# Performance work log

Hardware: AMD Instinct MI355X
Metric: run time of the kernel (lower is better)

## Reference

```python
import jax, jax.numpy as jnp
import numpy as np

H = 1024  # hidden_dim; GRU hidden size is H+1, embedding_dim = 2*H


def _bigru_scan(h0, Wih_f, Whh_f, bih_f, bhh_f, Wih_b, Whh_b, bih_b, bhh_b):
    """h0: (T, 2, H+1). Runs the per-token recurrence of AnswerSynthesisEncoder.

    At each step the torch code feeds the previous step's output y (2H+2,) back
    in as the GRU *input* x = y[:2H].reshape(2,H).sum(0), and uses the token
    embedding (+f_s,f_e) reshaped to (2, H+1) as the initial hidden state h_0
    of the bidirectional, seq_len=1 GRU. Since h_0 does not depend on the
    carry, the hidden-side gate preactivations are precomputed as one GEMM.
    """
    Hh = H + 1
    gh_f = h0[:, 0] @ Whh_f.T + bhh_f  # (T, 3*(H+1))
    gh_b = h0[:, 1] @ Whh_b.T + bhh_b

    def cell(x, h, gh, Wih, bih):
        gi = Wih @ x + bih
        i_r, i_z, i_n = jnp.split(gi, 3)
        h_r, h_z, h_n = jnp.split(gh, 3)
        r = jax.nn.sigmoid(i_r + h_r)
        z = jax.nn.sigmoid(i_z + h_z)
        n = jnp.tanh(i_n + r * h_n)
        return (1.0 - z) * n + z * h

    def step(y, inp):
        h0_t, ghf_t, ghb_t = inp
        x = y[: 2 * H].reshape(2, H).sum(axis=0)  # (H,)
        yf = cell(x, h0_t[0], ghf_t, Wih_f, bih_f)
        yb = cell(x, h0_t[1], ghb_t, Wih_b, bih_b)
        y_new = jnp.concatenate([yf, yb])  # (2H+2,)
        return y_new, y_new

    y0 = jnp.zeros(2 * Hh, dtype=h0.dtype)
    _, outs = jax.lax.scan(step, y0, (h0, gh_f, gh_b))  # (T, 2H+2)
    # final slice: reshape(2, H+1)[:, :H] per token -> concat of both halves' first H
    return jnp.concatenate([outs[:, :H], outs[:, Hh : Hh + H]], axis=1)  # (T, 2H)


def setup_inputs() -> dict:
    key = jax.random.key(0)
    ks = jax.random.split(key, 12)
    Hh = H + 1
    s = 0.02
    return {
        "e_q": jax.random.normal(ks[0], (512, 2 * H), jnp.float32),
        "e_p": jax.random.normal(ks[1], (4096, 2 * H), jnp.float32),
        "f_s": jax.random.uniform(ks[2], (4096, 1), jnp.float32),
        "f_e": jax.random.uniform(ks[3], (4096, 1), jnp.float32),
        "Wih_f": jax.random.normal(ks[4], (3 * Hh, H), jnp.float32) * s,
        "Whh_f": jax.random.normal(ks[5], (3 * Hh, Hh), jnp.float32) * s,
        "bih_f": jax.random.normal(ks[6], (3 * Hh,), jnp.float32) * s,
        "bhh_f": jax.random.normal(ks[7], (3 * Hh,), jnp.float32) * s,
        "Wih_b": jax.random.normal(ks[8], (3 * Hh, H), jnp.float32) * s,
        "Whh_b": jax.random.normal(ks[9], (3 * Hh, Hh), jnp.float32) * s,
        "bih_b": jax.random.normal(ks[10], (3 * Hh,), jnp.float32) * s,
        "bhh_b": jax.random.normal(ks[11], (3 * Hh,), jnp.float32) * s,
    }


def reference(e_q, e_p, f_s, f_e, Wih_f, Whh_f, bih_f, bhh_f, Wih_b, Whh_b, bih_b, bhh_b):
    Hh = H + 1
    # h_0 per passage token: cat([e_p_t, f_s_t, f_e_t]).reshape(2, H+1)
    h0_p = jnp.concatenate([e_p, f_s, f_e], axis=1).reshape(-1, 2, Hh)
    # h_0 per query token: cat([e_q_t, 0, 0]).reshape(2, H+1)
    zq = jnp.zeros((e_q.shape[0], 2), e_q.dtype)
    h0_q = jnp.concatenate([e_q, zq], axis=1).reshape(-1, 2, Hh)
    h_p = _bigru_scan(h0_p, Wih_f, Whh_f, bih_f, bhh_f, Wih_b, Whh_b, bih_b, bhh_b)
    h_q = _bigru_scan(h0_q, Wih_f, Whh_f, bih_f, bhh_f, Wih_b, Whh_b, bih_b, bhh_b)
    return (h_q, h_p)
```

## Files before the change

### kernel.cpp

```cpp
#include <hip/hip_runtime.h>
#include <stdint.h>


#define H   1024
#define HH  1025
#define N3  3075
#define TQ  512
#define TP  4096
#define MTOT 4608
#define GTOT 2050

typedef unsigned long long ull;

__device__ __forceinline__ float sigm(float x) { return 1.f / (1.f + __expf(-x)); }

__global__ __launch_bounds__(256, 2) void gh_gemm(
    const float* __restrict__ eq, const float* __restrict__ ep,
    const float* __restrict__ fs, const float* __restrict__ fe,
    const float* __restrict__ Whh_f, const float* __restrict__ bhh_f,
    const float* __restrict__ Whh_b, const float* __restrict__ bhh_b,
    float* __restrict__ ghf, float* __restrict__ ghb)
{
    const int dir = blockIdx.z;
    const float* W  = dir ? Whh_b : Whh_f;
    const float* bh = dir ? bhh_b : bhh_f;
    float* gh = dir ? ghb : ghf;
    const int n0 = blockIdx.x * 128;
    const int m0 = blockIdx.y * 128;

    __shared__ float As[16][132];
    __shared__ float Bs[16][132];

    float acc[8][8];
#pragma unroll
    for (int i = 0; i < 8; i++)
#pragma unroll
        for (int j = 0; j < 8; j++) acc[i][j] = 0.f;

    const int tid = threadIdx.x;
    const int tx = tid & 15, ty = tid >> 4;

    for (int k0 = 0; k0 < HH; k0 += 16) {
#pragma unroll
        for (int u = 0; u < 8; u++) {
            int lin = tid + 256 * u;
            int k = lin & 15;
            int m = lin >> 4;
            int gm = m0 + m;
            int gk = k0 + k;
            float v = 0.f;
            if (gk < HH) {
                bool isq = gm < TQ;
                const float* e = isq ? eq : ep;
                int t = isq ? gm : gm - TQ;
                if (dir == 0)            v = e[(size_t)t * 2048 + gk];
                else if (gk < 1023)      v = e[(size_t)t * 2048 + 1025 + gk];
                else if (!isq)           v = (gk == 1023) ? fs[t] : fe[t];
            }
            As[k][m] = v;
        }
#pragma unroll
        for (int u = 0; u < 8; u++) {
            int lin = tid + 256 * u;
            int k = lin & 15;
            int r = lin >> 4;
            int gr = n0 + r, gk = k0 + k;
            Bs[k][r] = (gr < N3 && gk < HH) ? W[(size_t)gr * HH + gk] : 0.f;
        }
        __syncthreads();
#pragma unroll
        for (int kk = 0; kk < 16; kk++) {
            float4 a0 = *(const float4*)&As[kk][ty * 4];
            float4 a1 = *(const float4*)&As[kk][64 + ty * 4];
            float4 b0 = *(const float4*)&Bs[kk][tx * 4];
            float4 b1 = *(const float4*)&Bs[kk][64 + tx * 4];
            float a[8] = {a0.x, a0.y, a0.z, a0.w, a1.x, a1.y, a1.z, a1.w};
            float b[8] = {b0.x, b0.y, b0.z, b0.w, b1.x, b1.y, b1.z, b1.w};
#pragma unroll
            for (int i = 0; i < 8; i++)
#pragma unroll
                for (int j = 0; j < 8; j++) acc[i][j] += a[i] * b[j];
        }
        __syncthreads();
    }
#pragma unroll
    for (int i = 0; i < 8; i++) {
        int gm = m0 + ((i < 4) ? (ty * 4 + i) : (64 + ty * 4 + i - 4));
#pragma unroll
        for (int j = 0; j < 8; j++) {
            int gr = n0 + ((j < 4) ? (tx * 4 + j) : (64 + tx * 4 + j - 4));
            if (gr < N3) gh[(size_t)gm * N3 + gr] = acc[i][j] + bh[gr];
        }
    }
}

__global__ __launch_bounds__(256, 1) void bigru_scan(
    const float* __restrict__ eq, const float* __restrict__ ep,
    const float* __restrict__ fs, const float* __restrict__ fe,
    const float* __restrict__ Wih_f, const float* __restrict__ bih_f,
    const float* __restrict__ Wih_b, const float* __restrict__ bih_b,
    const float* __restrict__ ghf, const float* __restrict__ ghb,
    ull* __restrict__ comm,
    float* __restrict__ out)
{
    __shared__ float xsh[2][2][1024];

    const int tid  = threadIdx.x;
    const int wave = tid >> 6;
    const int lane = tid & 63;
    const int gbase = blockIdx.x * 12 + wave * 3;

    float wreg[9][16];
    float breg[9];
    int   dre[3], je[3];
    bool  vale[3];
#pragma unroll
    for (int e = 0; e < 3; e++) {
        int g = gbase + e;
        bool v = (g < GTOT);
        int gc = v ? g : 0;
        int dir = gc / HH;
        int j = gc % HH;
        dre[e] = dir; je[e] = j; vale[e] = v;
        const float* Wih = dir ? Wih_b : Wih_f;
        const float* bih = dir ? bih_b : bih_f;
#pragma unroll
        for (int gate = 0; gate < 3; gate++) {
            const float* wr = Wih + (size_t)(gate * HH + j) * H;
#pragma unroll
            for (int i = 0; i < 4; i++) {
                float4 w4 = *(const float4*)(wr + i * 256 + lane * 4);
                wreg[e * 3 + gate][i * 4 + 0] = w4.x;
                wreg[e * 3 + gate][i * 4 + 1] = w4.y;
                wreg[e * 3 + gate][i * 4 + 2] = w4.z;
                wreg[e * 3 + gate][i * 4 + 3] = w4.w;
            }
            breg[e * 3 + gate] = bih[gate * HH + j];
        }
    }

    ull* commP = comm;
    ull* commQ = comm + 2 * GTOT;

    for (int t = 0; t < TP; t++) {
        const bool doq = (t < TQ);
        const int par = t & 1;

        float ghp[9], ghq[9], h0p[3], h0q[3];
#pragma unroll
        for (int e = 0; e < 3; e++) {
            const float* gh = dre[e] ? ghb : ghf;
            const int j = je[e];
            size_t basep = (size_t)(TQ + t) * N3;
            ghp[e * 3 + 0] = gh[basep + 0 * HH + j];
            ghp[e * 3 + 1] = gh[basep + 1 * HH + j];
            ghp[e * 3 + 2] = gh[basep + 2 * HH + j];
            if (dre[e] == 0) h0p[e] = ep[(size_t)t * 2048 + j];
            else h0p[e] = (j < 1023) ? ep[(size_t)t * 2048 + 1025 + j]
                                     : ((j == 1023) ? fs[t] : fe[t]);
            if (doq) {
                size_t baseq = (size_t)t * N3;
                ghq[e * 3 + 0] = gh[baseq + 0 * HH + j];
                ghq[e * 3 + 1] = gh[baseq + 1 * HH + j];
                ghq[e * 3 + 2] = gh[baseq + 2 * HH + j];
                if (dre[e] == 0) h0q[e] = eq[(size_t)t * 2048 + j];
                else h0q[e] = (j < 1023) ? eq[(size_t)t * 2048 + 1025 + j] : 0.f;
            } else { ghq[e*3+0]=ghq[e*3+1]=ghq[e*3+2]=0.f; h0q[e]=0.f; }
        }

        if (t == 0) {
#pragma unroll
            for (int u = 0; u < 4; u++) {
                int j = tid + 256 * u;
                xsh[par][0][j] = 0.f;
                xsh[par][1][j] = 0.f;
            }
        } else {
            const int slot = (t + 1) & 1;
            const unsigned tag = (unsigned)t;
            ull* cp = commP + slot * GTOT;
            ull* cq = commQ + slot * GTOT;
            int idx[8];
#pragma unroll
            for (int u = 0; u < 4; u++) {
                int j = tid + 256 * u;
                idx[2 * u]     = j;
                idx[2 * u + 1] = (j == 0) ? 1024 : (1025 + j - 1);
            }
            ull vp[8], vq[8];
#pragma unroll
            for (int u = 0; u < 8; u++)
                vp[u] = __hip_atomic_load(&cp[idx[u]], __ATOMIC_RELAXED, __HIP_MEMORY_SCOPE_AGENT);
            if (doq) {
#pragma unroll
                for (int u = 0; u < 8; u++)
                    vq[u] = __hip_atomic_load(&cq[idx[u]], __ATOMIC_RELAXED, __HIP_MEMORY_SCOPE_AGENT);
            }
#pragma unroll
            for (int u = 0; u < 8; u++) {
                while ((unsigned)(vp[u] >> 32) != tag) {
                    __builtin_amdgcn_s_sleep(1);
                    vp[u] = __hip_atomic_load(&cp[idx[u]], __ATOMIC_RELAXED, __HIP_MEMORY_SCOPE_AGENT);
                }
            }
#pragma unroll
            for (int u = 0; u < 4; u++) {
                int j = tid + 256 * u;
                xsh[par][0][j] = __uint_as_float((unsigned)vp[2 * u]) +
                                 __uint_as_float((unsigned)vp[2 * u + 1]);
            }
            if (doq) {
#pragma unroll
                for (int u = 0; u < 8; u++) {
                    while ((unsigned)(vq[u] >> 32) != tag) {
                        __builtin_amdgcn_s_sleep(1);
                        vq[u] = __hip_atomic_load(&cq[idx[u]], __ATOMIC_RELAXED, __HIP_MEMORY_SCOPE_AGENT);
                    }
                }
#pragma unroll
                for (int u = 0; u < 4; u++) {
                    int j = tid + 256 * u;
                    xsh[par][1][j] = __uint_as_float((unsigned)vq[2 * u]) +
                                     __uint_as_float((unsigned)vq[2 * u + 1]);
                }
            }
        }
        __syncthreads();

        float accp[9];
        {
            float x[16];
#pragma unroll
            for (int i = 0; i < 4; i++) {
                float4 x4 = *(const float4*)&xsh[par][0][i * 256 + lane * 4];
                x[i * 4 + 0] = x4.x; x[i * 4 + 1] = x4.y;
                x[i * 4 + 2] = x4.z; x[i * 4 + 3] = x4.w;
            }
#pragma unroll
            for (int r = 0; r < 9; r++) {
                float s = 0.f;
#pragma unroll
                for (int i = 0; i < 16; i++) s += wreg[r][i] * x[i];
                accp[r] = s;
            }
        }
#pragma unroll
        for (int r = 0; r < 9; r++) {
            float v = accp[r];
#pragma unroll
            for (int off = 32; off > 0; off >>= 1) v += __shfl_xor(v, off, 64);
            accp[r] = v + breg[r];
        }

        float accq[9];
        if (doq) {
            float x[16];
#pragma unroll
            for (int i = 0; i < 4; i++) {
                float4 x4 = *(const float4*)&xsh[par][1][i * 256 + lane * 4];
                x[i * 4 + 0] = x4.x; x[i * 4 + 1] = x4.y;
                x[i * 4 + 2] = x4.z; x[i * 4 + 3] = x4.w;
            }
#pragma unroll
            for (int r = 0; r < 9; r++) {
                float s = 0.f;
#pragma unroll
                for (int i = 0; i < 16; i++) s += wreg[r][i] * x[i];
#pragma unroll
                for (int off = 32; off > 0; off >>= 1) s += __shfl_xor(s, off, 64);
                accq[r] = s + breg[r];
            }
        }

        const ull tagout = ((ull)(unsigned)(t + 1)) << 32;
#pragma unroll
        for (int e = 0; e < 3; e++) {
            int g = gbase + e;
            {
                float r = sigm(accp[e * 3 + 0] + ghp[e * 3 + 0]);
                float z = sigm(accp[e * 3 + 1] + ghp[e * 3 + 1]);
                float n = tanhf(accp[e * 3 + 2] + r * ghp[e * 3 + 2]);
                float y = (1.f - z) * n + z * h0p[e];
                if (lane == 0 && vale[e]) {
                    ull pk = tagout | (ull)__float_as_uint(y);
                    __hip_atomic_store(&commP[(t & 1) * GTOT + g], pk,
                                       __ATOMIC_RELAXED, __HIP_MEMORY_SCOPE_AGENT);
                    if (je[e] < H)
                        out[(size_t)TQ * 2048 + (size_t)t * 2048 + dre[e] * H + je[e]] = y;
                }
            }
            if (doq) {
                float r = sigm(accq[e * 3 + 0] + ghq[e * 3 + 0]);
                float z = sigm(accq[e * 3 + 1] + ghq[e * 3 + 1]);
                float n = tanhf(accq[e * 3 + 2] + r * ghq[e * 3 + 2]);
                float y = (1.f - z) * n + z * h0q[e];
                if (lane == 0 && vale[e]) {
                    ull pk = tagout | (ull)__float_as_uint(y);
                    __hip_atomic_store(&commQ[(t & 1) * GTOT + g], pk,
                                       __ATOMIC_RELAXED, __HIP_MEMORY_SCOPE_AGENT);
                    if (je[e] < H)
                        out[(size_t)t * 2048 + dre[e] * H + je[e]] = y;
                }
            }
        }
    }
}

extern "C" void kernel_launch(void* const* d_in, const int* in_sizes, int n_in,
                              void* d_out, int out_size, void* d_ws, size_t ws_size,
                              hipStream_t stream) {
    const float* eq    = (const float*)d_in[0];
    const float* ep    = (const float*)d_in[1];
    const float* fs    = (const float*)d_in[2];
    const float* fe    = (const float*)d_in[3];
    const float* Wih_f = (const float*)d_in[4];
    const float* Whh_f = (const float*)d_in[5];
    const float* bih_f = (const float*)d_in[6];
    const float* bhh_f = (const float*)d_in[7];
    const float* Wih_b = (const float*)d_in[8];
    const float* Whh_b = (const float*)d_in[9];
    const float* bih_b = (const float*)d_in[10];
    const float* bhh_b = (const float*)d_in[11];
    float* out = (float*)d_out;

    const size_t ghElems = (size_t)MTOT * N3;
    float* ghf = (float*)d_ws;
    float* ghb = ghf + ghElems;
    size_t commOff = ((2 * ghElems * sizeof(float)) + 4095) & ~(size_t)4095;
    ull* comm = (ull*)((char*)d_ws + commOff);

    hipMemsetAsync(comm, 0, (size_t)4 * GTOT * sizeof(ull), stream);

    dim3 ggrid((N3 + 127) / 128, MTOT / 128, 2);
    gh_gemm<<<ggrid, 256, 0, stream>>>(eq, ep, fs, fe, Whh_f, bhh_f, Whh_b, bhh_b, ghf, ghb);

    bigru_scan<<<dim3(171), dim3(256), 0, stream>>>(
        eq, ep, fs, fe, Wih_f, bih_f, Wih_b, bih_b, ghf, ghb, comm, out);
}
```

Before: 16.66 ms.

## Prefetch next-step gate inputs, merge spin-waits, use fast tanh in GRU scan

Loads the precomputed hidden-gate preactivations and h0 values for step t+1 during step t, so global-load latency overlaps the matvec instead of sitting on the serial critical path. The per-element offsets become wave-uniform scalars via readfirstlane. The P and Q spin-waits are merged into one polling loop without s_sleep, the output stores are moved after both communication stores, and tanhf is replaced by an exp-based fast tanh. This trades some register pressure and a small amount of tanh accuracy (overflow handling for large inputs) for lower per-step latency.

```diff
diff --git a/kernel.cpp b/kernel.cpp
--- a/kernel.cpp
+++ b/kernel.cpp
@@ -9,10 +9,15 @@
 #define TP  4096
 #define MTOT 4608
 #define GTOT 2050
+#define GH_ELEMS (MTOT * N3)
 
 typedef unsigned long long ull;
 
 __device__ __forceinline__ float sigm(float x) { return 1.f / (1.f + __expf(-x)); }
+__device__ __forceinline__ float fast_tanh(float x) {
+    float e = __expf(2.f * x);
+    return (e - 1.f) / (e + 1.f);
+}
 
 __global__ __launch_bounds__(256, 2) void gh_gemm(
     const float* __restrict__ eq, const float* __restrict__ ep,
@@ -139,34 +144,49 @@
         }
     }
 
+    int sgh[3], sh0[3], sspec[3];
+#pragma unroll
+    for (int e = 0; e < 3; e++) {
+        sgh[e]   = __builtin_amdgcn_readfirstlane(dre[e] * GH_ELEMS + je[e]);
+        sh0[e]   = __builtin_amdgcn_readfirstlane(dre[e] ? (1025 + je[e]) : je[e]);
+        sspec[e] = __builtin_amdgcn_readfirstlane(
+                       (dre[e] && je[e] >= 1023) ? (je[e] - 1022) : 0);
+    }
+    const float* ghAll = ghf;
+
+    float ghcP[9], h0cP[3], ghcQ[9], h0cQ[3];
+
+    auto loadP = [&](int tt, float gh9[9], float h03[3]) {
+        size_t base = (size_t)(TQ + tt) * N3;
+#pragma unroll
+        for (int e = 0; e < 3; e++) {
+#pragma unroll
+            for (int gate = 0; gate < 3; gate++)
+                gh9[e * 3 + gate] = ghAll[base + (size_t)sgh[e] + gate * HH];
+            h03[e] = (sspec[e] == 0) ? ep[(size_t)tt * 2048 + sh0[e]]
+                   : (sspec[e] == 1) ? fs[tt] : fe[tt];
+        }
+    };
+    auto loadQ = [&](int tt, float gh9[9], float h03[3]) {
+        size_t base = (size_t)tt * N3;
+#pragma unroll
+        for (int e = 0; e < 3; e++) {
+#pragma unroll
+            for (int gate = 0; gate < 3; gate++)
+                gh9[e * 3 + gate] = ghAll[base + (size_t)sgh[e] + gate * HH];
+            h03[e] = (sspec[e] == 0) ? eq[(size_t)tt * 2048 + sh0[e]] : 0.f;
+        }
+    };
+
+    loadP(0, ghcP, h0cP);
+    loadQ(0, ghcQ, h0cQ);
+
     ull* commP = comm;
     ull* commQ = comm + 2 * GTOT;
 
     for (int t = 0; t < TP; t++) {
         const bool doq = (t < TQ);
         const int par = t & 1;
-
-        float ghp[9], ghq[9], h0p[3], h0q[3];
-#pragma unroll
-        for (int e = 0; e < 3; e++) {
-            const float* gh = dre[e] ? ghb : ghf;
-            const int j = je[e];
-            size_t basep = (size_t)(TQ + t) * N3;
-            ghp[e * 3 + 0] = gh[basep + 0 * HH + j];
-            ghp[e * 3 + 1] = gh[basep + 1 * HH + j];
-            ghp[e * 3 + 2] = gh[basep + 2 * HH + j];
-            if (dre[e] == 0) h0p[e] = ep[(size_t)t * 2048 + j];
-            else h0p[e] = (j < 1023) ? ep[(size_t)t * 2048 + 1025 + j]
-                                     : ((j == 1023) ? fs[t] : fe[t]);
-            if (doq) {
-                size_t baseq = (size_t)t * N3;
-                ghq[e * 3 + 0] = gh[baseq + 0 * HH + j];
-                ghq[e * 3 + 1] = gh[baseq + 1 * HH + j];
-                ghq[e * 3 + 2] = gh[baseq + 2 * HH + j];
-                if (dre[e] == 0) h0q[e] = eq[(size_t)t * 2048 + j];
-                else h0q[e] = (j < 1023) ? eq[(size_t)t * 2048 + 1025 + j] : 0.f;
-            } else { ghq[e*3+0]=ghq[e*3+1]=ghq[e*3+2]=0.f; h0q[e]=0.f; }
-        }
 
         if (t == 0) {
 #pragma unroll
@@ -196,11 +216,24 @@
                 for (int u = 0; u < 8; u++)
                     vq[u] = __hip_atomic_load(&cq[idx[u]], __ATOMIC_RELAXED, __HIP_MEMORY_SCOPE_AGENT);
             }
-#pragma unroll
-            for (int u = 0; u < 8; u++) {
-                while ((unsigned)(vp[u] >> 32) != tag) {
-                    __builtin_amdgcn_s_sleep(1);
-                    vp[u] = __hip_atomic_load(&cp[idx[u]], __ATOMIC_RELAXED, __HIP_MEMORY_SCOPE_AGENT);
+            bool done = false;
+            while (!done) {
+                done = true;
+#pragma unroll
+                for (int u = 0; u < 8; u++) {
+                    if ((unsigned)(vp[u] >> 32) != tag) {
+                        done = false;
+                        vp[u] = __hip_atomic_load(&cp[idx[u]], __ATOMIC_RELAXED, __HIP_MEMORY_SCOPE_AGENT);
+                    }
+                }
+                if (doq) {
+#pragma unroll
+                    for (int u = 0; u < 8; u++) {
+                        if ((unsigned)(vq[u] >> 32) != tag) {
+                            done = false;
+                            vq[u] = __hip_atomic_load(&cq[idx[u]], __ATOMIC_RELAXED, __HIP_MEMORY_SCOPE_AGENT);
+                        }
+                    }
                 }
             }
 #pragma unroll
@@ -211,13 +244,6 @@
             }
             if (doq) {
 #pragma unroll
-                for (int u = 0; u < 8; u++) {
-                    while ((unsigned)(vq[u] >> 32) != tag) {
-                        __builtin_amdgcn_s_sleep(1);
-                        vq[u] = __hip_atomic_load(&cq[idx[u]], __ATOMIC_RELAXED, __HIP_MEMORY_SCOPE_AGENT);
-                    }
-                }
-#pragma unroll
                 for (int u = 0; u < 4; u++) {
                     int j = tid + 256 * u;
                     xsh[par][1][j] = __uint_as_float((unsigned)vq[2 * u]) +
@@ -227,6 +253,12 @@
         }
         __syncthreads();
 
+        float ghnP[9], h0nP[3], ghnQ[9], h0nQ[3];
+        const bool ldn = (t + 1) < TP;
+        const bool ldq = (t + 1) < TQ;
+        if (ldn) loadP(t + 1, ghnP, h0nP);
+        if (ldq) loadQ(t + 1, ghnQ, h0nQ);
+
         float accp[9];
         {
             float x[16];
@@ -273,35 +305,55 @@
         }
 
         const ull tagout = ((ull)(unsigned)(t + 1)) << 32;
+        float yP[3], yQ[3];
 #pragma unroll
         for (int e = 0; e < 3; e++) {
-            int g = gbase + e;
-            {
-                float r = sigm(accp[e * 3 + 0] + ghp[e * 3 + 0]);
-                float z = sigm(accp[e * 3 + 1] + ghp[e * 3 + 1]);
-                float n = tanhf(accp[e * 3 + 2] + r * ghp[e * 3 + 2]);
-                float y = (1.f - z) * n + z * h0p[e];
+            float r = sigm(accp[e * 3 + 0] + ghcP[e * 3 + 0]);
+            float z = sigm(accp[e * 3 + 1] + ghcP[e * 3 + 1]);
+            float n = fast_tanh(accp[e * 3 + 2] + r * ghcP[e * 3 + 2]);
+            yP[e] = (1.f - z) * n + z * h0cP[e];
+            if (lane == 0 && vale[e]) {
+                ull pk = tagout | (ull)__float_as_uint(yP[e]);
+                __hip_atomic_store(&commP[par * GTOT + (gbase + e)], pk,
+                                   __ATOMIC_RELAXED, __HIP_MEMORY_SCOPE_AGENT);
+            }
+        }
+        if (doq) {
+#pragma unroll
+            for (int e = 0; e < 3; e++) {
+                float r = sigm(accq[e * 3 + 0] + ghcQ[e * 3 + 0]);
+                float z = sigm(accq[e * 3 + 1] + ghcQ[e * 3 + 1]);
+                float n = fast_tanh(accq[e * 3 + 2] + r * ghcQ[e * 3 + 2]);
+                yQ[e] = (1.f - z) * n + z * h0cQ[e];
                 if (lane == 0 && vale[e]) {
-                    ull pk = tagout | (ull)__float_as_uint(y);
-                    __hip_atomic_store(&commP[(t & 1) * GTOT + g], pk,
+                    ull pk = tagout | (ull)__float_as_uint(yQ[e]);
+                    __hip_atomic_store(&commQ[par * GTOT + (gbase + e)], pk,
                                        __ATOMIC_RELAXED, __HIP_MEMORY_SCOPE_AGENT);
-                    if (je[e] < H)
-                        out[(size_t)TQ * 2048 + (size_t)t * 2048 + dre[e] * H + je[e]] = y;
-                }
-            }
-            if (doq) {
-                float r = sigm(accq[e * 3 + 0] + ghq[e * 3 + 0]);
-                float z = sigm(accq[e * 3 + 1] + ghq[e * 3 + 1]);
-                float n = tanhf(accq[e * 3 + 2] + r * ghq[e * 3 + 2]);
-                float y = (1.f - z) * n + z * h0q[e];
-                if (lane == 0 && vale[e]) {
-                    ull pk = tagout | (ull)__float_as_uint(y);
-                    __hip_atomic_store(&commQ[(t & 1) * GTOT + g], pk,
-                                       __ATOMIC_RELAXED, __HIP_MEMORY_SCOPE_AGENT);
-                    if (je[e] < H)
-                        out[(size_t)t * 2048 + dre[e] * H + je[e]] = y;
-                }
-            }
+                }
+            }
+        }
+        if (lane == 0) {
+#pragma unroll
+            for (int e = 0; e < 3; e++) {
+                if (vale[e] && je[e] < H) {
+                    out[(size_t)TQ * 2048 + (size_t)t * 2048 + dre[e] * H + je[e]] = yP[e];
+                    if (doq)
+                        out[(size_t)t * 2048 + dre[e] * H + je[e]] = yQ[e];
+                }
+            }
+        }
+
+        if (ldn) {
+#pragma unroll
+            for (int i = 0; i < 9; i++) ghcP[i] = ghnP[i];
+#pragma unroll
+            for (int e = 0; e < 3; e++) h0cP[e] = h0nP[e];
+        }
+        if (ldq) {
+#pragma unroll
+            for (int i = 0; i < 9; i++) ghcQ[i] = ghnQ[i];
+#pragma unroll
+            for (int e = 0; e < 3; e++) h0cQ[e] = h0nQ[e];
         }
     }
 }
@@ -323,7 +375,7 @@
     const float* bhh_b = (const float*)d_in[11];
     float* out = (float*)d_out;
 
-    const size_t ghElems = (size_t)MTOT * N3;
+    const size_t ghElems = (size_t)GH_ELEMS;
     float* ghf = (float*)d_ws;
     float* ghb = ghf + ghElems;
     size_t commOff = ((2 * ghElems * sizeof(float)) + 4095) & ~(size_t)4095;
```

After: 14.59 ms. 1.14x faster.

## Split passage and query scans across waves and publish pre-summed inputs

Applied to the files above, without the earlier changes.

The persistent scan is restructured so that each wave owns one or two output units and runs on its own. There is no shared-memory staging and no block-level __syncthreads. Passage and query recurrences now run in separate block groups, each with its own comm buffer. The forward and backward halves are summed before publishing, which roughly halves the number of tagged atomic loads per step. The next step's gh and h0 values are prefetched while waiting on the spin flags, and tanhf is replaced by an exp-based fast tanh. In exchange the kernel launches more waves that spin on global memory, and the fast tanh adds some precision risk.

```diff
diff --git a/kernel.cpp b/kernel.cpp
--- a/kernel.cpp
+++ b/kernel.cpp
@@ -8,11 +8,24 @@
 #define TQ  512
 #define TP  4096
 #define MTOT 4608
-#define GTOT 2050
+#define GH_ELEMS ((size_t)MTOT * (size_t)N3)
+#define PBLK 257
+#define QBLK 129
+#define CSTRIDE 1040
 
 typedef unsigned long long ull;
 
 __device__ __forceinline__ float sigm(float x) { return 1.f / (1.f + __expf(-x)); }
+__device__ __forceinline__ float fast_tanh(float x) {
+    float e = __expf(2.f * x);
+    return (e - 1.f) / (e + 1.f);
+}
+__device__ __forceinline__ ull aload(const ull* p) {
+    return __hip_atomic_load((ull*)p, __ATOMIC_RELAXED, __HIP_MEMORY_SCOPE_AGENT);
+}
+__device__ __forceinline__ void astore(ull* p, ull v) {
+    __hip_atomic_store(p, v, __ATOMIC_RELAXED, __HIP_MEMORY_SCOPE_AGENT);
+}
 
 __global__ __launch_bounds__(256, 2) void gh_gemm(
     const float* __restrict__ eq, const float* __restrict__ ep,
@@ -94,215 +107,193 @@
     }
 }
 
-__global__ __launch_bounds__(256, 1) void bigru_scan(
+template <int NU>
+__device__ __forceinline__ void scan_impl(
+    int ubase, int lane, int nT,
+    const float* __restrict__ emb,
+    const float* __restrict__ fs,
+    const float* __restrict__ Wih_f, const float* __restrict__ bih_f,
+    const float* __restrict__ Wih_b, const float* __restrict__ bih_b,
+    const float* __restrict__ ghF,
+    const float* __restrict__ ghB,
+    ull* __restrict__ cm,
+    float* __restrict__ outc)
+{
+    const int NE = 2 * NU;
+    const int NR = 3 * NE;
+    ubase = __builtin_amdgcn_readfirstlane(ubase);
+
+    int  dir_[NE], row_[NE], h0col_[NE], h0mode_[NE];
+    bool val_[NE], st_[NE];
+#pragma unroll
+    for (int k = 0; k < NU; k++) {
+        int u = ubase + k;
+        if (u <= 1023)      { dir_[2*k]=0; row_[2*k]=u;    val_[2*k]=true;  st_[2*k]=true; }
+        else if (u == 1024) { dir_[2*k]=1; row_[2*k]=1023; val_[2*k]=true;  st_[2*k]=true; }
+        else                { dir_[2*k]=0; row_[2*k]=0;    val_[2*k]=false; st_[2*k]=false; }
+        if (u == 0)         { dir_[2*k+1]=0; row_[2*k+1]=1024; val_[2*k+1]=true;  st_[2*k+1]=false; }
+        else if (u <= 1023) { dir_[2*k+1]=1; row_[2*k+1]=u-1;  val_[2*k+1]=true;  st_[2*k+1]=true; }
+        else                { dir_[2*k+1]=0; row_[2*k+1]=0;    val_[2*k+1]=false; st_[2*k+1]=false; }
+    }
+#pragma unroll
+    for (int e = 0; e < NE; e++) {
+        dir_[e] = __builtin_amdgcn_readfirstlane(dir_[e]);
+        row_[e] = __builtin_amdgcn_readfirstlane(row_[e]);
+        if (dir_[e] == 0) { h0col_[e] = row_[e]; h0mode_[e] = 0; }
+        else if (row_[e] < 1023) { h0col_[e] = 1025 + row_[e]; h0mode_[e] = 0; }
+        else { h0col_[e] = 0; h0mode_[e] = 1; }
+    }
+
+    float wreg[NR][16];
+    float breg[NR];
+    const float* ghp_[NE];
+#pragma unroll
+    for (int e = 0; e < NE; e++) {
+        const float* W  = dir_[e] ? Wih_b : Wih_f;
+        const float* bb = dir_[e] ? bih_b : bih_f;
+        ghp_[e] = (dir_[e] ? ghB : ghF) + row_[e];
+#pragma unroll
+        for (int g = 0; g < 3; g++) {
+            const float* wr = W + (size_t)(g * HH + row_[e]) * H;
+#pragma unroll
+            for (int i = 0; i < 4; i++) {
+                float4 w4 = *(const float4*)(wr + i * 256 + lane * 4);
+                wreg[e*3+g][i*4+0] = w4.x; wreg[e*3+g][i*4+1] = w4.y;
+                wreg[e*3+g][i*4+2] = w4.z; wreg[e*3+g][i*4+3] = w4.w;
+            }
+            breg[e*3+g] = bb[g * HH + row_[e]];
+        }
+    }
+
+    float ghc[NR], h0c[NE];
+    auto ldgh = [&](int tt, float gh[], float h0[]) {
+        size_t base = (size_t)tt * N3;
+#pragma unroll
+        for (int e = 0; e < NE; e++) {
+#pragma unroll
+            for (int g = 0; g < 3; g++)
+                gh[e*3+g] = ghp_[e][base + g * HH];
+            h0[e] = (h0mode_[e] == 0) ? emb[(size_t)tt * 2048 + h0col_[e]]
+                                      : (fs ? fs[tt] : 0.f);
+        }
+    };
+    ldgh(0, ghc, h0c);
+
+    for (int t = 0; t < nT; ++t) {
+        ull v[17];
+        float x[16];
+        ull* wrs = cm + (t & 1) * CSTRIDE;
+        const ull* rd = cm + ((t + 1) & 1) * CSTRIDE;
+
+        if (t) {
+#pragma unroll
+            for (int i = 0; i < 4; i++)
+#pragma unroll
+                for (int m = 0; m < 4; m++)
+                    v[i*4+m] = aload(&rd[4*lane + 256*i + m]);
+            v[16] = aload(&rd[1024]);
+        }
+
+        float ghn[NR], h0n[NE];
+        const bool more = (t + 1) < nT;
+        if (more) ldgh(t + 1, ghn, h0n);
+
+        if (t) {
+            const unsigned tag = (unsigned)t;
+            for (;;) {
+                bool ok = true;
+#pragma unroll
+                for (int u2 = 0; u2 < 17; u2++) {
+                    if ((unsigned)(v[u2] >> 32) != tag) {
+                        ok = false;
+                        int slot = (u2 < 16) ? (4*lane + 256*(u2 >> 2) + (u2 & 3)) : 1024;
+                        v[u2] = aload(&rd[slot]);
+                    }
+                }
+                if (ok) break;
+            }
+#pragma unroll
+            for (int u2 = 0; u2 < 16; u2++) x[u2] = __uint_as_float((unsigned)v[u2]);
+        } else {
+#pragma unroll
+            for (int u2 = 0; u2 < 16; u2++) x[u2] = 0.f;
+        }
+
+        float acc[NR];
+#pragma unroll
+        for (int r = 0; r < NR; r++) {
+            float s = 0.f;
+#pragma unroll
+            for (int i = 0; i < 16; i++) s += wreg[r][i] * x[i];
+            acc[r] = s;
+        }
+#pragma unroll
+        for (int off = 32; off > 0; off >>= 1)
+#pragma unroll
+            for (int r = 0; r < NR; r++) acc[r] += __shfl_xor(acc[r], off, 64);
+
+        float y[NE];
+#pragma unroll
+        for (int e = 0; e < NE; e++) {
+            float rr = sigm(acc[e*3+0] + breg[e*3+0] + ghc[e*3+0]);
+            float zz = sigm(acc[e*3+1] + breg[e*3+1] + ghc[e*3+1]);
+            float nn = fast_tanh(acc[e*3+2] + breg[e*3+2] + rr * ghc[e*3+2]);
+            y[e] = (1.f - zz) * nn + zz * h0c[e];
+        }
+
+        if (lane == 0) {
+            const ull tagout = ((ull)(unsigned)(t + 1)) << 32;
+#pragma unroll
+            for (int k = 0; k < NU; k++) {
+                int u = ubase + k;
+                if (u <= 1024) {
+                    float xv = y[2*k] + ((u <= 1023) ? y[2*k+1] : 0.f);
+                    astore(&wrs[u], tagout | (ull)__float_as_uint(xv));
+                }
+            }
+#pragma unroll
+            for (int e = 0; e < NE; e++) {
+                if (val_[e] && st_[e]) {
+                    int col = dir_[e] ? (1024 + row_[e]) : row_[e];
+                    outc[(size_t)t * 2048 + col] = y[e];
+                }
+            }
+        }
+
+        if (more) {
+#pragma unroll
+            for (int r = 0; r < NR; r++) ghc[r] = ghn[r];
+#pragma unroll
+            for (int e = 0; e < NE; e++) h0c[e] = h0n[e];
+        }
+    }
+}
+
+__global__ __launch_bounds__(256, 2) void bigru_scan(
     const float* __restrict__ eq, const float* __restrict__ ep,
-    const float* __restrict__ fs, const float* __restrict__ fe,
+    const float* __restrict__ fs,
     const float* __restrict__ Wih_f, const float* __restrict__ bih_f,
     const float* __restrict__ Wih_b, const float* __restrict__ bih_b,
     const float* __restrict__ ghf, const float* __restrict__ ghb,
-    ull* __restrict__ comm,
-    float* __restrict__ out)
+    ull* __restrict__ comm, float* __restrict__ out)
 {
-    __shared__ float xsh[2][2][1024];
-
-    const int tid  = threadIdx.x;
-    const int wave = tid >> 6;
-    const int lane = tid & 63;
-    const int gbase = blockIdx.x * 12 + wave * 3;
-
-    float wreg[9][16];
-    float breg[9];
-    int   dre[3], je[3];
-    bool  vale[3];
-#pragma unroll
-    for (int e = 0; e < 3; e++) {
-        int g = gbase + e;
-        bool v = (g < GTOT);
-        int gc = v ? g : 0;
-        int dir = gc / HH;
-        int j = gc % HH;
-        dre[e] = dir; je[e] = j; vale[e] = v;
-        const float* Wih = dir ? Wih_b : Wih_f;
-        const float* bih = dir ? bih_b : bih_f;
-#pragma unroll
-        for (int gate = 0; gate < 3; gate++) {
-            const float* wr = Wih + (size_t)(gate * HH + j) * H;
-#pragma unroll
-            for (int i = 0; i < 4; i++) {
-                float4 w4 = *(const float4*)(wr + i * 256 + lane * 4);
-                wreg[e * 3 + gate][i * 4 + 0] = w4.x;
-                wreg[e * 3 + gate][i * 4 + 1] = w4.y;
-                wreg[e * 3 + gate][i * 4 + 2] = w4.z;
-                wreg[e * 3 + gate][i * 4 + 3] = w4.w;
-            }
-            breg[e * 3 + gate] = bih[gate * HH + j];
-        }
-    }
-
-    ull* commP = comm;
-    ull* commQ = comm + 2 * GTOT;
-
-    for (int t = 0; t < TP; t++) {
-        const bool doq = (t < TQ);
-        const int par = t & 1;
-
-        float ghp[9], ghq[9], h0p[3], h0q[3];
-#pragma unroll
-        for (int e = 0; e < 3; e++) {
-            const float* gh = dre[e] ? ghb : ghf;
-            const int j = je[e];
-            size_t basep = (size_t)(TQ + t) * N3;
-            ghp[e * 3 + 0] = gh[basep + 0 * HH + j];
-            ghp[e * 3 + 1] = gh[basep + 1 * HH + j];
-            ghp[e * 3 + 2] = gh[basep + 2 * HH + j];
-            if (dre[e] == 0) h0p[e] = ep[(size_t)t * 2048 + j];
-            else h0p[e] = (j < 1023) ? ep[(size_t)t * 2048 + 1025 + j]
-                                     : ((j == 1023) ? fs[t] : fe[t]);
-            if (doq) {
-                size_t baseq = (size_t)t * N3;
-                ghq[e * 3 + 0] = gh[baseq + 0 * HH + j];
-                ghq[e * 3 + 1] = gh[baseq + 1 * HH + j];
-                ghq[e * 3 + 2] = gh[baseq + 2 * HH + j];
-                if (dre[e] == 0) h0q[e] = eq[(size_t)t * 2048 + j];
-                else h0q[e] = (j < 1023) ? eq[(size_t)t * 2048 + 1025 + j] : 0.f;
-            } else { ghq[e*3+0]=ghq[e*3+1]=ghq[e*3+2]=0.f; h0q[e]=0.f; }
-        }
-
-        if (t == 0) {
-#pragma unroll
-            for (int u = 0; u < 4; u++) {
-                int j = tid + 256 * u;
-                xsh[par][0][j] = 0.f;
-                xsh[par][1][j] = 0.f;
-            }
-        } else {
-            const int slot = (t + 1) & 1;
-            const unsigned tag = (unsigned)t;
-            ull* cp = commP + slot * GTOT;
-            ull* cq = commQ + slot * GTOT;
-            int idx[8];
-#pragma unroll
-            for (int u = 0; u < 4; u++) {
-                int j = tid + 256 * u;
-                idx[2 * u]     = j;
-                idx[2 * u + 1] = (j == 0) ? 1024 : (1025 + j - 1);
-            }
-            ull vp[8], vq[8];
-#pragma unroll
-            for (int u = 0; u < 8; u++)
-                vp[u] = __hip_atomic_load(&cp[idx[u]], __ATOMIC_RELAXED, __HIP_MEMORY_SCOPE_AGENT);
-            if (doq) {
-#pragma unroll
-                for (int u = 0; u < 8; u++)
-                    vq[u] = __hip_atomic_load(&cq[idx[u]], __ATOMIC_RELAXED, __HIP_MEMORY_SCOPE_AGENT);
-            }
-#pragma unroll
-            for (int u = 0; u < 8; u++) {
-                while ((unsigned)(vp[u] >> 32) != tag) {
-                    __builtin_amdgcn_s_sleep(1);
-                    vp[u] = __hip_atomic_load(&cp[idx[u]], __ATOMIC_RELAXED, __HIP_MEMORY_SCOPE_AGENT);
-                }
-            }
-#pragma unroll
-            for (int u = 0; u < 4; u++) {
-                int j = tid + 256 * u;
-                xsh[par][0][j] = __uint_as_float((unsigned)vp[2 * u]) +
-                                 __uint_as_float((unsigned)vp[2 * u + 1]);
-            }
-            if (doq) {
-#pragma unroll
-                for (int u = 0; u < 8; u++) {
-                    while ((unsigned)(vq[u] >> 32) != tag) {
-                        __builtin_amdgcn_s_sleep(1);
-                        vq[u] = __hip_atomic_load(&cq[idx[u]], __ATOMIC_RELAXED, __HIP_MEMORY_SCOPE_AGENT);
-                    }
-                }
-#pragma unroll
-                for (int u = 0; u < 4; u++) {
-                    int j = tid + 256 * u;
-                    xsh[par][1][j] = __uint_as_float((unsigned)vq[2 * u]) +
-                                     __uint_as_float((unsigned)vq[2 * u + 1]);
-                }
-            }
-        }
-        __syncthreads();
-
-        float accp[9];
-        {
-            float x[16];
-#pragma unroll
-            for (int i = 0; i < 4; i++) {
-                float4 x4 = *(const float4*)&xsh[par][0][i * 256 + lane * 4];
-                x[i * 4 + 0] = x4.x; x[i * 4 + 1] = x4.y;
-                x[i * 4 + 2] = x4.z; x[i * 4 + 3] = x4.w;
-            }
-#pragma unroll
-            for (int r = 0; r < 9; r++) {
-                float s = 0.f;
-#pragma unroll
-                for (int i = 0; i < 16; i++) s += wreg[r][i] * x[i];
-                accp[r] = s;
-            }
-        }
-#pragma unroll
-        for (int r = 0; r < 9; r++) {
-            float v = accp[r];
-#pragma unroll
-            for (int off = 32; off > 0; off >>= 1) v += __shfl_xor(v, off, 64);
-            accp[r] = v + breg[r];
-        }
-
-        float accq[9];
-        if (doq) {
-            float x[16];
-#pragma unroll
-            for (int i = 0; i < 4; i++) {
-                float4 x4 = *(const float4*)&xsh[par][1][i * 256 + lane * 4];
-                x[i * 4 + 0] = x4.x; x[i * 4 + 1] = x4.y;
-                x[i * 4 + 2] = x4.z; x[i * 4 + 3] = x4.w;
-            }
-#pragma unroll
-            for (int r = 0; r < 9; r++) {
-                float s = 0.f;
-#pragma unroll
-                for (int i = 0; i < 16; i++) s += wreg[r][i] * x[i];
-#pragma unroll
-                for (int off = 32; off > 0; off >>= 1) s += __shfl_xor(s, off, 64);
-                accq[r] = s + breg[r];
-            }
-        }
-
-        const ull tagout = ((ull)(unsigned)(t + 1)) << 32;
-#pragma unroll
-        for (int e = 0; e < 3; e++) {
-            int g = gbase + e;
-            {
-                float r = sigm(accp[e * 3 + 0] + ghp[e * 3 + 0]);
-                float z = sigm(accp[e * 3 + 1] + ghp[e * 3 + 1]);
-                float n = tanhf(accp[e * 3 + 2] + r * ghp[e * 3 + 2]);
-                float y = (1.f - z) * n + z * h0p[e];
-                if (lane == 0 && vale[e]) {
-                    ull pk = tagout | (ull)__float_as_uint(y);
-                    __hip_atomic_store(&commP[(t & 1) * GTOT + g], pk,
-                                       __ATOMIC_RELAXED, __HIP_MEMORY_SCOPE_AGENT);
-                    if (je[e] < H)
-                        out[(size_t)TQ * 2048 + (size_t)t * 2048 + dre[e] * H + je[e]] = y;
-                }
-            }
-            if (doq) {
-                float r = sigm(accq[e * 3 + 0] + ghq[e * 3 + 0]);
-                float z = sigm(accq[e * 3 + 1] + ghq[e * 3 + 1]);
-                float n = tanhf(accq[e * 3 + 2] + r * ghq[e * 3 + 2]);
-                float y = (1.f - z) * n + z * h0q[e];
-                if (lane == 0 && vale[e]) {
-                    ull pk = tagout | (ull)__float_as_uint(y);
-                    __hip_atomic_store(&commQ[(t & 1) * GTOT + g], pk,
-                                       __ATOMIC_RELAXED, __HIP_MEMORY_SCOPE_AGENT);
-                    if (je[e] < H)
-                        out[(size_t)t * 2048 + dre[e] * H + je[e]] = y;
-                }
-            }
-        }
+    const int wave = threadIdx.x >> 6;
+    const int lane = threadIdx.x & 63;
+    if ((int)blockIdx.x < PBLK) {
+        int ub = blockIdx.x * 4 + wave;
+        if (ub > 1024) return;
+        scan_impl<1>(ub, lane, TP, ep, fs,
+                     Wih_f, bih_f, Wih_b, bih_b,
+                     ghf + (size_t)TQ * N3, ghb + (size_t)TQ * N3,
+                     comm, out + (size_t)TQ * 2048);
+    } else {
+        int qi = (blockIdx.x - PBLK) * 4 + wave;
+        int ub = 2 * qi;
+        if (ub > 1024) return;
+        scan_impl<2>(ub, lane, TQ, eq, nullptr,
+                     Wih_f, bih_f, Wih_b, bih_b,
+                     ghf, ghb,
+                     comm + 2 * CSTRIDE, out);
     }
 }
 
@@ -323,17 +314,16 @@
     const float* bhh_b = (const float*)d_in[11];
     float* out = (float*)d_out;
 
-    const size_t ghElems = (size_t)MTOT * N3;
     float* ghf = (float*)d_ws;
-    float* ghb = ghf + ghElems;
-    size_t commOff = ((2 * ghElems * sizeof(float)) + 4095) & ~(size_t)4095;
+    float* ghb = ghf + GH_ELEMS;
+    size_t commOff = ((2 * GH_ELEMS * sizeof(float)) + 4095) & ~(size_t)4095;
     ull* comm = (ull*)((char*)d_ws + commOff);
 
-    hipMemsetAsync(comm, 0, (size_t)4 * GTOT * sizeof(ull), stream);
+    hipMemsetAsync(comm, 0, (size_t)4 * CSTRIDE * sizeof(ull), stream);
 
     dim3 ggrid((N3 + 127) / 128, MTOT / 128, 2);
     gh_gemm<<<ggrid, 256, 0, stream>>>(eq, ep, fs, fe, Whh_f, bhh_f, Whh_b, bhh_b, ghf, ghb);
 
-    bigru_scan<<<dim3(171), dim3(256), 0, stream>>>(
-        eq, ep, fs, fe, Wih_f, bih_f, Wih_b, bih_b, ghf, ghb, comm, out);
-}
+    bigru_scan<<<dim3(PBLK + QBLK), dim3(256), 0, stream>>>(
+        eq, ep, fs, Wih_f, bih_f, Wih_b, bih_b, ghf, ghb, comm, out);
+}
```

Result: slower. 34.69 ms (+108.2%).
